# Optimization experiments

Hardware: AMD Instinct MI355X
Metric: run time of the kernel (lower is better)

The kernel has to match this reference:

```python
import jax, jax.numpy as jnp
import numpy as np

D_MODEL = 1024
NUM_HEADS = 16
HEAD_DIM = D_MODEL // NUM_HEADS
BATCH = 4
SEQ = 2048


def circulant(x, c, b):
    # Circulant linear layer via FFT: y = irfft(rfft(x) * rfft(c)) + b
    # x: (..., d), c: (d,), b: (d,)
    d = c.shape[0]
    y = jnp.fft.irfft(jnp.fft.rfft(x, axis=-1) * jnp.fft.rfft(c), n=d, axis=-1)
    return y + b


def setup_inputs() -> dict:
    key = jax.random.key(0)
    ks = jax.random.split(key, 9)
    scale = 1.0 / np.sqrt(D_MODEL)
    inp = {
        "x": jax.random.normal(ks[0], (BATCH, SEQ, D_MODEL), dtype=jnp.float32),
        "wq_c": jax.random.normal(ks[1], (D_MODEL,), dtype=jnp.float32) * scale,
        "wq_b": jnp.zeros((D_MODEL,), dtype=jnp.float32),
        "wk_c": jax.random.normal(ks[2], (D_MODEL,), dtype=jnp.float32) * scale,
        "wk_b": jnp.zeros((D_MODEL,), dtype=jnp.float32),
        "wv_c": jax.random.normal(ks[3], (D_MODEL,), dtype=jnp.float32) * scale,
        "wv_b": jnp.zeros((D_MODEL,), dtype=jnp.float32),
        "wo_c": jax.random.normal(ks[4], (D_MODEL,), dtype=jnp.float32) * scale,
        "wo_b": jnp.zeros((D_MODEL,), dtype=jnp.float32),
    }
    return inp


def reference(x, wq_c, wq_b, wk_c, wk_b, wv_c, wv_b, wo_c, wo_b):
    bs, seq_len, dm = x.shape
    Q = circulant(x, wq_c, wq_b)  # (B, S, D)
    K = circulant(x, wk_c, wk_b)
    V = circulant(x, wv_c, wv_b)
    Q = Q.reshape(bs, seq_len, NUM_HEADS, HEAD_DIM)
    K = K.reshape(bs, seq_len, NUM_HEADS, HEAD_DIM)
    V = V.reshape(bs, seq_len, NUM_HEADS, HEAD_DIM)
    scale = HEAD_DIM ** (-0.5)
    attn_logits = jnp.einsum("bqhd,bkhd->bhqk", Q, K) * scale  # (B, H, S, S)
    attn_weights = jax.nn.softmax(attn_logits, axis=-1)
    out_heads = jnp.einsum("bhqk,bkhd->bqhd", attn_weights, V)
    out_merge = out_heads.reshape(bs, seq_len, dm)
    out = circulant(out_merge, wo_c, wo_b)
    return out
```

## Files before the change

kernel.cpp:

```cpp
#include <hip/hip_runtime.h>
#include <hip/hip_bf16.h>

#define D_MODEL 1024
#define NUM_HEADS 16
#define HEAD_DIM 64
#define BATCH 4
#define SEQ 2048
#define MROWS (BATCH * SEQ)

using f32x4  = __attribute__((ext_vector_type(4))) float;
using bf16x8 = __attribute__((ext_vector_type(8))) short;
using short4v = __attribute__((ext_vector_type(4))) short;

__device__ inline unsigned short f2bf(float f) {
    __hip_bfloat16 h = __float2bfloat16(f);
    return *reinterpret_cast<unsigned short*>(&h);
}

__device__ inline void gld_lds16(const unsigned short* g, unsigned short* l) {
    __builtin_amdgcn_global_load_lds(
        (const __attribute__((address_space(1))) unsigned int*)g,
        (__attribute__((address_space(3))) unsigned int*)l, 16, 0, 0);
}

#define QSCALE 0.18033688011112042f

__global__ __launch_bounds__(256) void build_w(
    const float* __restrict__ cq, const float* __restrict__ ck,
    const float* __restrict__ cv, const float* __restrict__ co,
    const float* __restrict__ bq, const float* __restrict__ bk,
    const float* __restrict__ bv, const float* __restrict__ bo,
    unsigned short* __restrict__ Wt, float* __restrict__ bias)
{
    const int n = blockIdx.x;
    const int sel = n >> 10, nl = n & 1023;
    const float* c  = sel == 0 ? cq : sel == 1 ? ck : sel == 2 ? cv : co;
    const float* bb = sel == 0 ? bq : sel == 1 ? bk : sel == 2 ? bv : bo;
    const float sc = (sel == 0) ? QSCALE : 1.0f;
    const int t = threadIdx.x;
    ushort4 o;
    o.x = f2bf(sc * c[(nl - (4*t + 0)) & 1023]);
    o.y = f2bf(sc * c[(nl - (4*t + 1)) & 1023]);
    o.z = f2bf(sc * c[(nl - (4*t + 2)) & 1023]);
    o.w = f2bf(sc * c[(nl - (4*t + 3)) & 1023]);
    ((ushort4*)(Wt + (size_t)n * 1024))[t] = o;
    if (t == 0) bias[n] = sc * bb[nl];
}

__global__ __launch_bounds__(256) void xcast(
    const float* __restrict__ x, unsigned short* __restrict__ xb)
{
    const size_t i = (size_t)blockIdx.x * 1024 + threadIdx.x * 4;
    float4 v = *(const float4*)(x + i);
    ushort4 o;
    o.x = f2bf(v.x); o.y = f2bf(v.y); o.z = f2bf(v.z); o.w = f2bf(v.w);
    *(ushort4*)(xb + i) = o;
}

template <int OUT_MODE>
__global__ __launch_bounds__(256, 3) void gemm_circ(
    const unsigned short* __restrict__ A,
    const unsigned short* __restrict__ Bt,
    const float* __restrict__ bias,
    unsigned short* __restrict__ Qb, unsigned short* __restrict__ Kb,
    unsigned short* __restrict__ Vt, float* __restrict__ Cf)
{
    __shared__ unsigned short As[128 * 64];
    __shared__ unsigned short Bs[128 * 64];
    const int t = threadIdx.x;
    const int w = t >> 6, lane = t & 63;
    const int quad = lane >> 4, l16 = lane & 15;
    const int m0 = blockIdx.x * 128;
    const int n0 = blockIdx.y * 128;
    const int wm = (w & 1) * 64, wn = (w >> 1) * 64;

    f32x4 acc[4][4];
#pragma unroll
    for (int i = 0; i < 4; ++i)
#pragma unroll
        for (int j = 0; j < 4; ++j) acc[i][j] = (f32x4){0.f, 0.f, 0.f, 0.f};

    for (int k0 = 0; k0 < 1024; k0 += 64) {
        __syncthreads();
#pragma unroll
        for (int j = 0; j < 4; ++j) {
            const int s = j * 4 + w;
            const int i = s * 64 + lane;
            const int r = i >> 3;
            const int c = (i & 7) ^ (r & 7);
            gld_lds16(A  + (size_t)(m0 + r) * 1024 + k0 + c * 8, &As[s * 512]);
            gld_lds16(Bt + (size_t)(n0 + r) * 1024 + k0 + c * 8, &Bs[s * 512]);
        }
        __syncthreads();

#pragma unroll
        for (int kk = 0; kk < 2; ++kk) {
            bf16x8 af[4], bfr[4];
#pragma unroll
            for (int i = 0; i < 4; ++i) {
                const int r = wm + i * 16 + l16;
                const int slot = r * 8 + ((kk * 4 + quad) ^ (r & 7));
                af[i] = *(const bf16x8*)&As[slot * 8];
            }
#pragma unroll
            for (int j = 0; j < 4; ++j) {
                const int r = wn + j * 16 + l16;
                const int slot = r * 8 + ((kk * 4 + quad) ^ (r & 7));
                bfr[j] = *(const bf16x8*)&Bs[slot * 8];
            }
#pragma unroll
            for (int i = 0; i < 4; ++i)
#pragma unroll
                for (int j = 0; j < 4; ++j)
                    acc[i][j] = __builtin_amdgcn_mfma_f32_16x16x32_bf16(
                        af[i], bfr[j], acc[i][j], 0, 0, 0);
        }
    }

#pragma unroll
    for (int i = 0; i < 4; ++i) {
        const int gm = m0 + wm + i * 16 + quad * 4;
#pragma unroll
        for (int j = 0; j < 4; ++j) {
            const int gn = n0 + wn + j * 16 + l16;
            const float bv = bias[gn];
            if (OUT_MODE == 1) {
#pragma unroll
                for (int rr = 0; rr < 4; ++rr)
                    Cf[(size_t)(gm + rr) * 1024 + gn] = acc[i][j][rr] + bv;
            } else {
                const int sel = gn >> 10;
                if (sel == 0) {
#pragma unroll
                    for (int rr = 0; rr < 4; ++rr)
                        Qb[(size_t)(gm + rr) * 1024 + gn] = f2bf(acc[i][j][rr] + bv);
                } else if (sel == 1) {
                    const int col = gn & 1023;
#pragma unroll
                    for (int rr = 0; rr < 4; ++rr)
                        Kb[(size_t)(gm + rr) * 1024 + col] = f2bf(acc[i][j][rr] + bv);
                } else {
                    const int d = gn & 1023;
                    const int head = d >> 6, dl = d & 63;
                    const int b = gm >> 11, key = gm & 2047;
                    ushort4 vv;
                    vv.x = f2bf(acc[i][j][0] + bv);
                    vv.y = f2bf(acc[i][j][1] + bv);
                    vv.z = f2bf(acc[i][j][2] + bv);
                    vv.w = f2bf(acc[i][j][3] + bv);
                    *(ushort4*)&Vt[((size_t)((b * 16 + head) * 64 + dl)) * 2048 + key] = vv;
                }
            }
        }
    }
}

__global__ __launch_bounds__(256, 4) void attn_mfma(
    const unsigned short* __restrict__ Qb, const unsigned short* __restrict__ Kb,
    const unsigned short* __restrict__ Vt, unsigned short* __restrict__ O)
{
    __shared__ unsigned short Ks[2][64 * 64];
    __shared__ unsigned short Vs[2][64 * 64];

    const int t = threadIdx.x;
    const int w = t >> 6, lane = t & 63;
    const int quad = lane >> 4, l16 = lane & 15;
    const int bh = blockIdx.x;
    const int b = bh >> 4, head = bh & 15;
    const int qbase = blockIdx.y * 128 + w * 32;

    bf16x8 qa[2][2];
#pragma unroll
    for (int s = 0; s < 2; ++s)
#pragma unroll
        for (int h = 0; h < 2; ++h) {
            size_t off = (size_t)(b * SEQ + qbase + s*16 + l16) * D_MODEL
                       + head * HEAD_DIM + h*32 + quad*8;
            qa[s][h] = *(const bf16x8*)(Qb + off);
        }

    f32x4 acc[2][4];
#pragma unroll
    for (int s = 0; s < 2; ++s)
#pragma unroll
        for (int dt = 0; dt < 4; ++dt) acc[s][dt] = (f32x4){0.f,0.f,0.f,0.f};
    float lp[2] = {0.f, 0.f};

    const size_t kbase  = (size_t)(b * SEQ) * D_MODEL + head * HEAD_DIM;
    const size_t vtbase = (size_t)((b * NUM_HEADS + head) * HEAD_DIM) * SEQ;

#pragma unroll
    for (int j = 0; j < 2; ++j) {
        const int seg = j * 4 + w;
        const int i = seg * 64 + lane;
        const int r = i >> 3;
        const int ck = (i & 7) ^ ((r & 3) | ((r >> 1) & 4));
        const int cv = (i & 7) ^ (r & 7);
        gld_lds16(Kb + kbase + (size_t)r * D_MODEL + ck * 8, &Ks[0][seg * 512]);
        gld_lds16(Vt + vtbase + (size_t)r * SEQ + cv * 8, &Vs[0][seg * 512]);
    }

    int ib = 0;
    for (int kb = 0; kb < SEQ; kb += 64, ib ^= 1) {
        __syncthreads();

        if (kb + 64 < SEQ) {
#pragma unroll
            for (int j = 0; j < 2; ++j) {
                const int seg = j * 4 + w;
                const int i = seg * 64 + lane;
                const int r = i >> 3;
                const int ck = (i & 7) ^ ((r & 3) | ((r >> 1) & 4));
                const int cv = (i & 7) ^ (r & 7);
                gld_lds16(Kb + kbase + (size_t)(kb + 64 + r) * D_MODEL + ck * 8,
                          &Ks[ib ^ 1][seg * 512]);
                gld_lds16(Vt + vtbase + (size_t)r * SEQ + kb + 64 + cv * 8,
                          &Vs[ib ^ 1][seg * 512]);
            }
        }

        bf16x8 kf[2][2][2];
#pragma unroll
        for (int kh = 0; kh < 2; ++kh)
#pragma unroll
            for (int m = 0; m < 2; ++m) {
                const int r = kh * 32 + ((l16 >> 2) << 3) + m * 4 + (l16 & 3);
                const int sg = (r & 3) | ((r >> 1) & 4);
#pragma unroll
                for (int h = 0; h < 2; ++h) {
                    const int cc = (h * 4 + quad) ^ sg;
                    kf[kh][m][h] = *(const bf16x8*)&Ks[ib][(r * 8 + cc) * 8];
                }
            }

#pragma unroll
        for (int kh = 0; kh < 2; ++kh) {
            bf16x8 pf[2];
#pragma unroll
            for (int s = 0; s < 2; ++s) {
                f32x4 st0 = (f32x4){0.f,0.f,0.f,0.f};
                f32x4 st1 = (f32x4){0.f,0.f,0.f,0.f};
#pragma unroll
                for (int h = 0; h < 2; ++h) {
                    st0 = __builtin_amdgcn_mfma_f32_16x16x32_bf16(
                        kf[kh][0][h], qa[s][h], st0, 0, 0, 0);
                    st1 = __builtin_amdgcn_mfma_f32_16x16x32_bf16(
                        kf[kh][1][h], qa[s][h], st1, 0, 0, 0);
                }
                float p0 = __builtin_amdgcn_exp2f(st0[0]);
                float p1 = __builtin_amdgcn_exp2f(st0[1]);
                float p2 = __builtin_amdgcn_exp2f(st0[2]);
                float p3 = __builtin_amdgcn_exp2f(st0[3]);
                float p4 = __builtin_amdgcn_exp2f(st1[0]);
                float p5 = __builtin_amdgcn_exp2f(st1[1]);
                float p6 = __builtin_amdgcn_exp2f(st1[2]);
                float p7 = __builtin_amdgcn_exp2f(st1[3]);
                lp[s] += ((p0 + p1) + (p2 + p3)) + ((p4 + p5) + (p6 + p7));
                __hip_bfloat162 w0 = __float22bfloat162_rn(make_float2(p0, p1));
                __hip_bfloat162 w1 = __float22bfloat162_rn(make_float2(p2, p3));
                __hip_bfloat162 w2 = __float22bfloat162_rn(make_float2(p4, p5));
                __hip_bfloat162 w3 = __float22bfloat162_rn(make_float2(p6, p7));
                union { bf16x8 v; unsigned int u[4]; } pu;
                pu.u[0] = *reinterpret_cast<unsigned int*>(&w0);
                pu.u[1] = *reinterpret_cast<unsigned int*>(&w1);
                pu.u[2] = *reinterpret_cast<unsigned int*>(&w2);
                pu.u[3] = *reinterpret_cast<unsigned int*>(&w3);
                pf[s] = pu.v;
            }

#pragma unroll
            for (int dt = 0; dt < 4; ++dt) {
                const int r = dt * 16 + l16;
                const int cv = (kh * 4 + quad) ^ (r & 7);
                bf16x8 vf = *(const bf16x8*)&Vs[ib][(r * 8 + cv) * 8];
#pragma unroll
                for (int s = 0; s < 2; ++s)
                    acc[s][dt] = __builtin_amdgcn_mfma_f32_16x16x32_bf16(
                        pf[s], vf, acc[s][dt], 0, 0, 0);
            }
        }
    }

#pragma unroll
    for (int s = 0; s < 2; ++s) {
        lp[s] += __shfl_xor(lp[s], 16);
        lp[s] += __shfl_xor(lp[s], 32);
    }

#pragma unroll
    for (int s = 0; s < 2; ++s)
#pragma unroll
        for (int rr = 0; rr < 4; ++rr) {
            float denom = __shfl(lp[s], quad * 4 + rr);
            float inv = 1.0f / denom;
            int q = qbase + s*16 + quad*4 + rr;
            unsigned short* orow = O + (size_t)(b * SEQ + q) * D_MODEL + head * HEAD_DIM + l16;
#pragma unroll
            for (int dt = 0; dt < 4; ++dt) orow[dt*16] = f2bf(acc[s][dt][rr] * inv);
        }
}

extern "C" void kernel_launch(void* const* d_in, const int* in_sizes, int n_in,
                              void* d_out, int out_size, void* d_ws, size_t ws_size,
                              hipStream_t stream) {
    const float* x    = (const float*)d_in[0];
    const float* wq_c = (const float*)d_in[1];
    const float* wq_b = (const float*)d_in[2];
    const float* wk_c = (const float*)d_in[3];
    const float* wk_b = (const float*)d_in[4];
    const float* wv_c = (const float*)d_in[5];
    const float* wv_b = (const float*)d_in[6];
    const float* wo_c = (const float*)d_in[7];
    const float* wo_b = (const float*)d_in[8];
    float* out = (float*)d_out;

    char* ws = (char*)d_ws;
    unsigned short* Wt   = (unsigned short*)(ws);
    float*          bias = (float*)(ws + ((size_t)8  << 20));
    unsigned short* xb   = (unsigned short*)(ws + ((size_t)10 << 20));
    unsigned short* Qb   = (unsigned short*)(ws + ((size_t)26 << 20));
    unsigned short* Kb   = (unsigned short*)(ws + ((size_t)42 << 20));
    unsigned short* Vt   = (unsigned short*)(ws + ((size_t)58 << 20));
    unsigned short* Ob   = (unsigned short*)(ws + ((size_t)74 << 20));

    build_w<<<4096, 256, 0, stream>>>(wq_c, wk_c, wv_c, wo_c,
                                      wq_b, wk_b, wv_b, wo_b, Wt, bias);
    xcast<<<MROWS, 256, 0, stream>>>(x, xb);
    gemm_circ<0><<<dim3(64, 24), 256, 0, stream>>>(xb, Wt, bias, Qb, Kb, Vt, nullptr);
    attn_mfma<<<dim3(BATCH * NUM_HEADS, SEQ / 128), 256, 0, stream>>>(Qb, Kb, Vt, Ob);
    gemm_circ<1><<<dim3(64, 8), 256, 0, stream>>>(Ob, Wt + (size_t)3072 * 1024,
                                                  bias + 3072, nullptr, nullptr, nullptr, out);
}
```

Before: 253.6 us.

## Replace QKV projection GEMM with 256x256-tile 512-thread double-buffered kernel

Adds a new GEMM kernel for the fused QKV projection that uses 256x256 output tiles with 8 waves, double-buffered LDS filled by direct global-to-LDS loads, XOR-swizzled layout, and MFMA phases split so prefetch of the next K tile overlaps compute. Larger tiles raise arithmetic intensity and cut redundant global reads compared with the previous 128-wide tile kernel. In exchange it uses 128KB LDS per block and many accumulator registers, and launches only 384 blocks, which may limit occupancy and leave CUs partly idle on the last wave.

```diff
diff --git a/kernel.cpp b/kernel.cpp
--- a/kernel.cpp
+++ b/kernel.cpp
@@ -22,6 +22,13 @@
         (const __attribute__((address_space(1))) unsigned int*)g,
         (__attribute__((address_space(3))) unsigned int*)l, 16, 0, 0);
 }
+
+__device__ inline void block_bar() {
+    asm volatile("" ::: "memory");
+    __builtin_amdgcn_s_barrier();
+    asm volatile("" ::: "memory");
+}
+#define WAIT_VM0() asm volatile("s_waitcnt vmcnt(0)" ::: "memory")
 
 #define QSCALE 0.18033688011112042f
 
@@ -150,6 +157,185 @@
                     vv.w = f2bf(acc[i][j][3] + bv);
                     *(ushort4*)&Vt[((size_t)((b * 16 + head) * 64 + dl)) * 2048 + key] = vv;
                 }
+            }
+        }
+    }
+}
+
+__global__ __launch_bounds__(512, 2) void gemm_big(
+    const unsigned short* __restrict__ A,
+    const unsigned short* __restrict__ Bt,
+    const float* __restrict__ bias,
+    unsigned short* __restrict__ Qb, unsigned short* __restrict__ Kb,
+    unsigned short* __restrict__ Vt)
+{
+    __shared__ unsigned short Ls[2][4 * 8192];
+
+    const int t = threadIdx.x;
+    const int w = t >> 6, lane = t & 63;
+    const int quad = lane >> 4, l16 = lane & 15;
+    const int wm = w >> 2, wn = w & 3;
+    const int n0 = blockIdx.x * 256;
+    const int m0 = blockIdx.y * 256;
+
+    const int r0 = t >> 3,        c0 = (t & 7) ^ (r0 & 7);
+    const int i1 = 512 + t;
+    const int r1 = i1 >> 3,       c1 = (i1 & 7) ^ (r1 & 7);
+    const int d0 = (w * 64) * 8;
+    const int d1 = (512 + w * 64) * 8;
+
+    f32x4 acc[8][4];
+#pragma unroll
+    for (int i = 0; i < 8; ++i)
+#pragma unroll
+        for (int j = 0; j < 4; ++j) acc[i][j] = (f32x4){0.f, 0.f, 0.f, 0.f};
+
+    bf16x8 af[4][2], bf0[2][2], bf1[2][2];
+    const int bu = 2 + (wn >> 1);
+    const int rb = (wn & 1) * 64;
+    const int cx = l16 & 7;
+
+#pragma unroll
+    for (int u = 0; u < 2; ++u) {
+        gld_lds16(A  + (size_t)(m0 + u * 128 + r0) * 1024 + c0 * 8, &Ls[0][u * 8192 + d0]);
+        gld_lds16(A  + (size_t)(m0 + u * 128 + r1) * 1024 + c1 * 8, &Ls[0][u * 8192 + d1]);
+    }
+#pragma unroll
+    for (int u = 0; u < 2; ++u) {
+        gld_lds16(Bt + (size_t)(n0 + u * 128 + r0) * 1024 + c0 * 8, &Ls[0][(2 + u) * 8192 + d0]);
+        gld_lds16(Bt + (size_t)(n0 + u * 128 + r1) * 1024 + c1 * 8, &Ls[0][(2 + u) * 8192 + d1]);
+    }
+    WAIT_VM0();
+    block_bar();
+
+    int p = 0;
+    for (int kt = 0; kt < 16; ++kt, p ^= 1) {
+        const unsigned short* LA = &Ls[p][wm * 8192];
+        const unsigned short* LB = &Ls[p][bu * 8192];
+        const int k1 = (kt + 1) * 64;
+        const bool pref = (kt + 1 < 16);
+
+        if (pref) {
+#pragma unroll
+            for (int u = 0; u < 2; ++u) {
+                gld_lds16(A + (size_t)(m0 + u * 128 + r0) * 1024 + k1 + c0 * 8,
+                          &Ls[p ^ 1][u * 8192 + d0]);
+                gld_lds16(A + (size_t)(m0 + u * 128 + r1) * 1024 + k1 + c1 * 8,
+                          &Ls[p ^ 1][u * 8192 + d1]);
+            }
+        }
+#pragma unroll
+        for (int fi = 0; fi < 4; ++fi) {
+            const int r = fi * 16 + l16;
+#pragma unroll
+            for (int kk = 0; kk < 2; ++kk)
+                af[fi][kk] = *(const bf16x8*)&LA[(r * 8 + ((kk * 4 + quad) ^ cx)) * 8];
+        }
+#pragma unroll
+        for (int fj = 0; fj < 2; ++fj) {
+            const int r = rb + fj * 16 + l16;
+#pragma unroll
+            for (int kk = 0; kk < 2; ++kk)
+                bf0[fj][kk] = *(const bf16x8*)&LB[(r * 8 + ((kk * 4 + quad) ^ cx)) * 8];
+        }
+        __builtin_amdgcn_s_setprio(1);
+#pragma unroll
+        for (int fi = 0; fi < 4; ++fi)
+#pragma unroll
+            for (int fj = 0; fj < 2; ++fj)
+#pragma unroll
+                for (int kk = 0; kk < 2; ++kk)
+                    acc[fi][fj] = __builtin_amdgcn_mfma_f32_16x16x32_bf16(
+                        af[fi][kk], bf0[fj][kk], acc[fi][fj], 0, 0, 0);
+        __builtin_amdgcn_s_setprio(0);
+
+        if (pref) {
+#pragma unroll
+            for (int u = 0; u < 2; ++u) {
+                gld_lds16(Bt + (size_t)(n0 + u * 128 + r0) * 1024 + k1 + c0 * 8,
+                          &Ls[p ^ 1][(2 + u) * 8192 + d0]);
+                gld_lds16(Bt + (size_t)(n0 + u * 128 + r1) * 1024 + k1 + c1 * 8,
+                          &Ls[p ^ 1][(2 + u) * 8192 + d1]);
+            }
+        }
+#pragma unroll
+        for (int fj = 0; fj < 2; ++fj) {
+            const int r = rb + 32 + fj * 16 + l16;
+#pragma unroll
+            for (int kk = 0; kk < 2; ++kk)
+                bf1[fj][kk] = *(const bf16x8*)&LB[(r * 8 + ((kk * 4 + quad) ^ cx)) * 8];
+        }
+        __builtin_amdgcn_s_setprio(1);
+#pragma unroll
+        for (int fi = 0; fi < 4; ++fi)
+#pragma unroll
+            for (int fj = 0; fj < 2; ++fj)
+#pragma unroll
+                for (int kk = 0; kk < 2; ++kk)
+                    acc[fi][2 + fj] = __builtin_amdgcn_mfma_f32_16x16x32_bf16(
+                        af[fi][kk], bf1[fj][kk], acc[fi][2 + fj], 0, 0, 0);
+        __builtin_amdgcn_s_setprio(0);
+
+#pragma unroll
+        for (int fi = 0; fi < 4; ++fi) {
+            const int r = 64 + fi * 16 + l16;
+#pragma unroll
+            for (int kk = 0; kk < 2; ++kk)
+                af[fi][kk] = *(const bf16x8*)&LA[(r * 8 + ((kk * 4 + quad) ^ cx)) * 8];
+        }
+        __builtin_amdgcn_s_setprio(1);
+#pragma unroll
+        for (int fi = 0; fi < 4; ++fi)
+#pragma unroll
+            for (int fj = 0; fj < 2; ++fj)
+#pragma unroll
+                for (int kk = 0; kk < 2; ++kk)
+                    acc[4 + fi][fj] = __builtin_amdgcn_mfma_f32_16x16x32_bf16(
+                        af[fi][kk], bf0[fj][kk], acc[4 + fi][fj], 0, 0, 0);
+        __builtin_amdgcn_s_setprio(0);
+
+        __builtin_amdgcn_s_setprio(1);
+#pragma unroll
+        for (int fi = 0; fi < 4; ++fi)
+#pragma unroll
+            for (int fj = 0; fj < 2; ++fj)
+#pragma unroll
+                for (int kk = 0; kk < 2; ++kk)
+                    acc[4 + fi][2 + fj] = __builtin_amdgcn_mfma_f32_16x16x32_bf16(
+                        af[fi][kk], bf1[fj][kk], acc[4 + fi][2 + fj], 0, 0, 0);
+        __builtin_amdgcn_s_setprio(0);
+
+        WAIT_VM0();
+        block_bar();
+    }
+
+#pragma unroll
+    for (int i = 0; i < 8; ++i) {
+        const int gm = m0 + wm * 128 + i * 16 + quad * 4;
+#pragma unroll
+        for (int j = 0; j < 4; ++j) {
+            const int gn = n0 + wn * 64 + j * 16 + l16;
+            const float bv = bias[gn];
+            const int sel = gn >> 10;
+            if (sel == 0) {
+#pragma unroll
+                for (int rr = 0; rr < 4; ++rr)
+                    Qb[(size_t)(gm + rr) * 1024 + gn] = f2bf(acc[i][j][rr] + bv);
+            } else if (sel == 1) {
+                const int col = gn & 1023;
+#pragma unroll
+                for (int rr = 0; rr < 4; ++rr)
+                    Kb[(size_t)(gm + rr) * 1024 + col] = f2bf(acc[i][j][rr] + bv);
+            } else {
+                const int d = gn & 1023;
+                const int head = d >> 6, dl = d & 63;
+                const int b = gm >> 11, key = gm & 2047;
+                ushort4 vv;
+                vv.x = f2bf(acc[i][j][0] + bv);
+                vv.y = f2bf(acc[i][j][1] + bv);
+                vv.z = f2bf(acc[i][j][2] + bv);
+                vv.w = f2bf(acc[i][j][3] + bv);
+                *(ushort4*)&Vt[((size_t)((b * 16 + head) * 64 + dl)) * 2048 + key] = vv;
             }
         }
     }
@@ -326,7 +512,7 @@
     build_w<<<4096, 256, 0, stream>>>(wq_c, wk_c, wv_c, wo_c,
                                       wq_b, wk_b, wv_b, wo_b, Wt, bias);
     xcast<<<MROWS, 256, 0, stream>>>(x, xb);
-    gemm_circ<0><<<dim3(64, 24), 256, 0, stream>>>(xb, Wt, bias, Qb, Kb, Vt, nullptr);
+    gemm_big<<<dim3(12, 32), 512, 0, stream>>>(xb, Wt, bias, Qb, Kb, Vt);
     attn_mfma<<<dim3(BATCH * NUM_HEADS, SEQ / 128), 256, 0, stream>>>(Qb, Kb, Vt, Ob);
     gemm_circ<1><<<dim3(64, 8), 256, 0, stream>>>(Ob, Wt + (size_t)3072 * 1024,
                                                   bias + 3072, nullptr, nullptr, nullptr, out);
```

New measurement: 260.0 us. +2.5%, slower.
